# Kernel optimization log

Measured on AMD Instinct MI355X. Metric: run time of the kernel, lower is better.

## Reference

```python
import jax, jax.numpy as jnp
import numpy as np

B = 1_048_576
W = 64  # hidden width
N_FREQ = 6   # 3 dims * 6 freqs * (sin,cos) = 36
K_BLOB = 4   # one-blob bins per dim


def _freq_embed(p):
    # [B,3] -> [B,36]
    freqs = 2.0 ** jnp.arange(N_FREQ, dtype=p.dtype)
    ang = jnp.pi * p[:, :, None] * freqs  # [B,3,6]
    return jnp.concatenate([jnp.sin(ang), jnp.cos(ang)], axis=-1).reshape(p.shape[0], 3 * 2 * N_FREQ)


def _sph(d):
    # unit-square parameterization of a direction, [B,3] -> [B,2]
    d = d / (jnp.linalg.norm(d, axis=-1, keepdims=True) + 1e-8)
    u = jnp.arctan2(d[:, 1], d[:, 0]) / (2.0 * jnp.pi) + 0.5
    v = jnp.arccos(jnp.clip(d[:, 2], -1.0 + 1e-6, 1.0 - 1e-6)) / jnp.pi
    return jnp.stack([u, v], axis=-1)


def _one_blob(x, k=K_BLOB):
    # x in [0,1], [B,D] -> [B,D*k] Gaussian one-blob encoding
    centers = (jnp.arange(k, dtype=x.dtype) + 0.5) / k
    sigma = 1.0 / k
    g = jnp.exp(-0.5 * ((x[..., None] - centers) / sigma) ** 2)  # [B,D,k]
    return g.reshape(x.shape[0], -1)


def _encode(p, wi, n, alpha, beta, r):
    ones = jnp.ones((p.shape[0], 2), dtype=p.dtype)
    return jnp.concatenate([
        _freq_embed(p),                      # 36
        _one_blob(_sph(wi)),                 # 8
        _one_blob(_sph(n)),                  # 8
        _one_blob(1.0 - jnp.exp(-r)),        # 4
        alpha, beta,                         # 6
        ones,                                # 2 (implicit bias)
    ], axis=-1)                              # -> [B,64]


def _mlp(x, Ws):
    h = x
    for Wk in Ws[:-1]:
        h = jax.nn.relu(h @ Wk.T)
    return h @ Ws[-1].T  # [B,3]


def setup_inputs() -> dict:
    key = jax.random.key(0)
    ks = jax.random.split(key, 13)
    p = jax.random.normal(ks[0], (B, 3), jnp.float32)
    wi = jax.random.normal(ks[1], (B, 3), jnp.float32)
    n = jax.random.normal(ks[2], (B, 3), jnp.float32)
    alpha = jax.random.uniform(ks[3], (B, 3), jnp.float32)
    beta = jax.random.uniform(ks[4], (B, 3), jnp.float32)
    r = jax.random.uniform(ks[5], (B, 1), jnp.float32)
    s = 1.0 / np.sqrt(W)
    weights = {}
    for i in range(6):
        weights[f"W{i}"] = jax.random.normal(ks[6 + i], (W, W), jnp.float32) * s
    weights["W6"] = jax.random.normal(ks[12], (3, W), jnp.float32) * s
    return dict(p=p, wi=wi, n=n, alpha=alpha, beta=beta, r=r, **weights)


def reference(p, wi, n, alpha, beta, r, W0, W1, W2, W3, W4, W5, W6):
    x = _encode(p, wi, n, alpha, beta, r)
    out = _mlp(x, [W0, W1, W2, W3, W4, W5, W6])
    return out * (alpha + beta)  # reflectance factorization
```

## Files before the change

kernel.cpp:

```cpp
#include <hip/hip_runtime.h>


typedef _Float16 f16;
typedef f16 f16x2 __attribute__((ext_vector_type(2)));
typedef f16 f16x4 __attribute__((ext_vector_type(4)));
typedef f16 f16x8 __attribute__((ext_vector_type(8)));
typedef float f32x4 __attribute__((ext_vector_type(4)));

#define MFMA32(A, B, C) __builtin_amdgcn_mfma_f32_16x16x32_f16(A, B, C, 0, 0, 0)
#define LDS_FENCE() __asm__ volatile("" ::: "memory")

static constexpr int TILES = 4;
static constexpr int WAVES = 8;
static constexpr int BLOCK = WAVES * 64;
static constexpr int SPB   = WAVES * 64;

static constexpr int    WUNITS   = 50;
static constexpr int    WCHUNKS  = WUNITS * 64;
static constexpr size_t WS_BYTES = (size_t)WCHUNKS * 16;
static constexpr int    HUNITS   = 48;
static constexpr int    HCHUNKS  = HUNITS * 64;
static constexpr int    LDS_W    = HUNITS * 1024;

__host__ __device__ __forceinline__ int tau(int x) {
    return (x & 32) + ((x & 7) >> 2) * 16 + ((x >> 3) & 3) * 4 + (x & 3);
}

__device__ __forceinline__ f16x2 pkh(float a, float b) {
    return __builtin_bit_cast(f16x2, __builtin_amdgcn_cvt_pkrtz(a, b));
}

__device__ __forceinline__ f16x4 cat22(f16x2 a, f16x2 b) {
    return __builtin_shufflevector(a, b, 0, 1, 2, 3);
}

__device__ __forceinline__ f16x8 cat44(f16x4 a, f16x4 b) {
    return __builtin_shufflevector(a, b, 0, 1, 2, 3, 4, 5, 6, 7);
}

__device__ __forceinline__ f16x4 pack4(f32x4 v) {
    f16x2 a = pkh(v[0], v[1]);
    f16x2 b = pkh(v[2], v[3]);
    return cat22(a, b);
}

__device__ __forceinline__ float fast_atan2_rev(float y, float x) {
    const float ax = __builtin_fabsf(x), ay = __builtin_fabsf(y);
    const float mx = fmaxf(ax, ay), mn = fminf(ax, ay);
    const float a = mn * __builtin_amdgcn_rcpf(fmaxf(mx, 1e-30f));
    const float s = a * a;
    float r = a * (0.99997726f + s * (-0.33262347f + s * (0.19354346f +
              s * (-0.11643287f + s * (0.05265332f - s * 0.01172120f)))));
    if (ay > ax) r = 1.5707963268f - r;
    if (x < 0.0f) r = 3.1415926536f - r;
    r = (y < 0.0f) ? -r : r;
    return r * 0.15915494309189535f;
}

__device__ __forceinline__ float fast_acos(float x) {
    const float ax = __builtin_fabsf(x);
    const float t = __builtin_amdgcn_sqrtf(1.0f - ax);
    const float p = t * (1.5707288f + ax * (-0.2121144f +
                    ax * (0.0742610f - ax * 0.0187293f)));
    return (x < 0.0f) ? (3.1415926536f - p) : p;
}

__device__ __forceinline__ void blob4(float x, float* out) {
    const float dx = x - 0.125f;
    const float E0 = __expf(-8.0f * dx * dx);
    const float R  = __expf(4.0f * dx);
    const float t1 = R * 0.60653066f;
    const float t2 = R * 0.22313016f;
    const float t3 = R * 0.082084999f;
    out[0] = E0;
    out[1] = E0 * t1;
    out[2] = out[1] * t2;
    out[3] = out[2] * t3;
}

__device__ __forceinline__ f16x8 make_wchunk(
    int c, const float* __restrict__ W0, const float* __restrict__ W1,
    const float* __restrict__ W2, const float* __restrict__ W3,
    const float* __restrict__ W4, const float* __restrict__ W5,
    const float* __restrict__ W6)
{
    const int lane2 = c & 63;
    const int unit  = c >> 6;
    const int q = lane2 >> 4, m = lane2 & 15;
    f16x8 v;
    if (unit < 48) {
        const int l = unit >> 3, kt = (unit & 7) >> 2, mt = unit & 3;
        const float* Ws[6] = {W0, W1, W2, W3, W4, W5};
        const float* __restrict__ Wl = Ws[l];
#pragma unroll
        for (int j = 0; j < 8; ++j) {
            const int x = kt * 32 + q * 8 + j;
            const int src = (l == 0) ? x : tau(x);
            v[j] = (f16)Wl[(mt * 16 + m) * 64 + src];
        }
    } else {
        const int kt = unit - 48;
#pragma unroll
        for (int j = 0; j < 8; ++j) {
            const int src = tau(kt * 32 + q * 8 + j);
            v[j] = (m < 3) ? (f16)W6[m * 64 + src] : (f16)0.0f;
        }
    }
    return v;
}

__global__ __launch_bounds__(256, 1) void pack_weights_kernel(
    const float* __restrict__ W0, const float* __restrict__ W1,
    const float* __restrict__ W2, const float* __restrict__ W3,
    const float* __restrict__ W4, const float* __restrict__ W5,
    const float* __restrict__ W6, f16* __restrict__ ws)
{
    const int c = (int)blockIdx.x * 256 + threadIdx.x;
    if (c >= WCHUNKS) return;
    *(f16x8*)(ws + (size_t)c * 8) = make_wchunk(c, W0, W1, W2, W3, W4, W5, W6);
}

__device__ __forceinline__ void async_ld16(const void* g, void* l) {
    __builtin_amdgcn_global_load_lds(
        (const __attribute__((address_space(1))) void*)g,
        (__attribute__((address_space(3))) void*)l,
        16, 0, 0);
}

template<int PACKED>
__global__ __launch_bounds__(BLOCK, 4) void nrc_mlp_kernel(
    const float* __restrict__ P,  const float* __restrict__ WI,
    const float* __restrict__ NV, const float* __restrict__ AL,
    const float* __restrict__ BE, const float* __restrict__ RR,
    const f16*   __restrict__ ws,
    const float* __restrict__ W0, const float* __restrict__ W1,
    const float* __restrict__ W2, const float* __restrict__ W3,
    const float* __restrict__ W4, const float* __restrict__ W5,
    const float* __restrict__ W6, float* __restrict__ Out)
{
    __shared__ __attribute__((aligned(16))) unsigned char smem[LDS_W];

    const int tid  = threadIdx.x;
    const int lane = tid & 63;
    const int w    = tid >> 6;
    const int q    = lane >> 4;
    const int m    = lane & 15;
    unsigned char* const hb = smem + w * 2048;

    const int wave_base = (int)blockIdx.x * SPB + w * 64;

    f16x8 w6f0, w6f1;
    if (PACKED) {
        w6f0 = *(const f16x8*)(ws + (size_t)(HCHUNKS + lane) * 8);
        w6f1 = *(const f16x8*)(ws + (size_t)(HCHUNKS + 64 + lane) * 8);
    } else {
        w6f0 = make_wchunk(HCHUNKS + lane,      W0, W1, W2, W3, W4, W5, W6);
        w6f1 = make_wchunk(HCHUNKS + 64 + lane, W0, W1, W2, W3, W4, W5, W6);
    }

    f16x2 hf[32];
    float ab0, ab1, ab2;

    {
        const int s = wave_base + lane;

        float pv[3], wv[3], nv[3], av[3], bv[3];
#pragma unroll
        for (int d = 0; d < 3; ++d) {
            pv[d] = P [s * 3 + d];
            wv[d] = WI[s * 3 + d];
            nv[d] = NV[s * 3 + d];
            av[d] = AL[s * 3 + d];
            bv[d] = BE[s * 3 + d];
        }
        const float rv = RR[s];

#pragma unroll
        for (int d = 0; d < 3; ++d) {
            float sA[6], cA[6];
            const float fr = __builtin_amdgcn_fractf(pv[d] * 0.5f);
            sA[0] = __builtin_amdgcn_sinf(fr);
            cA[0] = __builtin_amdgcn_cosf(fr);
#pragma unroll
            for (int k = 1; k < 6; ++k) {
                const float s2 = sA[k-1] * sA[k-1];
                const float sc = sA[k-1] * cA[k-1];
                cA[k] = fmaf(-2.0f, s2, 1.0f);
                sA[k] = sc + sc;
            }
            hf[d * 6 + 0] = pkh(sA[0], sA[1]);
            hf[d * 6 + 1] = pkh(sA[2], sA[3]);
            hf[d * 6 + 2] = pkh(sA[4], sA[5]);
            hf[d * 6 + 3] = pkh(cA[0], cA[1]);
            hf[d * 6 + 4] = pkh(cA[2], cA[3]);
            hf[d * 6 + 5] = pkh(cA[4], cA[5]);
        }
#pragma unroll
        for (int which = 0; which < 2; ++which) {
            const float* dv = (which == 0) ? wv : nv;
            const int ho = 18 + which * 4;
            const float nr = __builtin_amdgcn_sqrtf(dv[0]*dv[0] + dv[1]*dv[1] + dv[2]*dv[2]) + 1e-8f;
            const float u  = fast_atan2_rev(dv[1], dv[0]) + 0.5f;
            float zc = dv[2] * __builtin_amdgcn_rcpf(nr);
            zc = fminf(fmaxf(zc, -1.0f + 1e-6f), 1.0f - 1e-6f);
            const float vv = fast_acos(zc) * 0.3183098861837907f;
            float ob[8];
            blob4(u,  &ob[0]);
            blob4(vv, &ob[4]);
            hf[ho + 0] = pkh(ob[0], ob[1]);
            hf[ho + 1] = pkh(ob[2], ob[3]);
            hf[ho + 2] = pkh(ob[4], ob[5]);
            hf[ho + 3] = pkh(ob[6], ob[7]);
        }
        {
            float ob[4];
            blob4(1.0f - __expf(-rv), ob);
            hf[26] = pkh(ob[0], ob[1]);
            hf[27] = pkh(ob[2], ob[3]);
        }
        hf[28] = pkh(av[0], av[1]);
        hf[29] = pkh(av[2], bv[0]);
        hf[30] = pkh(bv[1], bv[2]);
        hf[31] = pkh(1.0f, 1.0f);

        ab0 = av[0] + bv[0];
        ab1 = av[1] + bv[1];
        ab2 = av[2] + bv[2];
    }

    const int te = lane >> 4;
    f16x8 bf[TILES][2];
#pragma unroll
    for (int pass = 0; pass < TILES; ++pass) {
        if (te == pass) {
            unsigned char* const tb = hb + m * 128;
#pragma unroll
            for (int g = 0; g < 8; ++g) {
                const int slot0 = (4 * g + 4 * m) & 31;
                *(f16x8*)(tb + slot0 * 4) =
                    cat44(cat22(hf[g*4 + 0], hf[g*4 + 1]),
                          cat22(hf[g*4 + 2], hf[g*4 + 3]));
            }
        }
        LDS_FENCE();
#pragma unroll
        for (int kt = 0; kt < 2; ++kt) {
            const int s0 = (16 * kt + 4 * q + 4 * m) & 31;
            bf[pass][kt] = *(const f16x8*)(hb + m * 128 + s0 * 4);
        }
        LDS_FENCE();
    }

    __syncthreads();

    if (PACKED) {
#pragma unroll
        for (int i = 0; i < HCHUNKS / BLOCK; ++i) {
            const int c = i * BLOCK + tid;
            async_ld16(ws + (size_t)c * 8, smem + c * 16);
        }
    } else {
#pragma unroll
        for (int i = 0; i < HCHUNKS / BLOCK; ++i) {
            const int c = i * BLOCK + tid;
            *(f16x8*)(smem + c * 16) = make_wchunk(c, W0, W1, W2, W3, W4, W5, W6);
        }
    }
    __syncthreads();

    const f16x4 zero4 = {(f16)0.0f, (f16)0.0f, (f16)0.0f, (f16)0.0f};
    const f32x4 ZF = {0.0f, 0.0f, 0.0f, 0.0f};
    unsigned char* const wb = smem + lane * 16;

    __builtin_amdgcn_s_setprio(1);

#pragma unroll
    for (int layer = 0; layer < 6; ++layer) {
        f16x8 wa[8];
#pragma unroll
        for (int f = 0; f < 8; ++f)
            wa[f] = *(const f16x8*)(wb + (layer * 8 + f) * 1024);

#pragma unroll
        for (int t = 0; t < TILES; ++t) {
            f32x4 acc[4];
#pragma unroll
            for (int mt = 0; mt < 4; ++mt) {
                f32x4 z = MFMA32(wa[mt], bf[t][0], ZF);
                z = MFMA32(wa[4 + mt], bf[t][1], z);
                acc[mt] = z;
            }
            f16x4 pk[4];
#pragma unroll
            for (int mt = 0; mt < 4; ++mt)
                pk[mt] = __builtin_elementwise_max(pack4(acc[mt]), zero4);
            bf[t][0] = cat44(pk[0], pk[1]);
            bf[t][1] = cat44(pk[2], pk[3]);
        }
    }

    {
#pragma unroll
        for (int t = 0; t < TILES; ++t) {
            f32x4 z = MFMA32(w6f0, bf[t][0], ZF);
            z = MFMA32(w6f1, bf[t][1], z);
            const int src = t * 16 + m;
            const float s0 = __shfl(ab0, src);
            const float s1 = __shfl(ab1, src);
            const float s2 = __shfl(ab2, src);
            if (lane < 16) {
                const int s = wave_base + t * 16 + m;
                float* o = Out + s * 3;
                o[0] = z[0] * s0;
                o[1] = z[1] * s1;
                o[2] = z[2] * s2;
            }
        }
    }
    __builtin_amdgcn_s_setprio(0);
}

extern "C" void kernel_launch(void* const* d_in, const int* in_sizes, int n_in,
                              void* d_out, int out_size, void* d_ws, size_t ws_size,
                              hipStream_t stream) {
    (void)n_in; (void)out_size;
    const float* P  = (const float*)d_in[0];
    const float* WI = (const float*)d_in[1];
    const float* NV = (const float*)d_in[2];
    const float* AL = (const float*)d_in[3];
    const float* BE = (const float*)d_in[4];
    const float* RR = (const float*)d_in[5];
    const float* W0 = (const float*)d_in[6];
    const float* W1 = (const float*)d_in[7];
    const float* W2 = (const float*)d_in[8];
    const float* W3 = (const float*)d_in[9];
    const float* W4 = (const float*)d_in[10];
    const float* W5 = (const float*)d_in[11];
    const float* W6 = (const float*)d_in[12];
    f16*   ws  = (f16*)d_ws;
    float* Out = (float*)d_out;

    const int Bn = in_sizes[0] / 3;
    const int grid = Bn / SPB;

    if (ws_size >= WS_BYTES) {
        hipLaunchKernelGGL(pack_weights_kernel, dim3((WCHUNKS + 255) / 256),
                           dim3(256), 0, stream, W0, W1, W2, W3, W4, W5, W6, ws);
        hipLaunchKernelGGL((nrc_mlp_kernel<1>), dim3(grid), dim3(BLOCK), 0, stream,
                           P, WI, NV, AL, BE, RR, ws,
                           W0, W1, W2, W3, W4, W5, W6, Out);
    } else {
        hipLaunchKernelGGL((nrc_mlp_kernel<0>), dim3(grid), dim3(BLOCK), 0, stream,
                           P, WI, NV, AL, BE, RR, ws,
                           W0, W1, W2, W3, W4, W5, W6, Out);
    }
}
```

Baseline: 153.5 us.

## Split block into producer and consumer waves to overlap encoding with MLP

Waves 0-3 now compute the input encoding for the next round while waves 4-7 run the MFMA MLP on the previous round, with an LDS staging buffer and block barriers handing tiles across. Each block processes 4 rounds of 256 samples instead of 512 samples once, so the weight load to LDS is amortized over more samples. The alpha+beta scale is re-read from global memory at output time instead of being shuffled. In exchange, only half the waves issue MFMAs, each round adds four block-wide barriers, LDS use grows by 16 KB, and the grid shrinks.

```diff
diff --git a/kernel.cpp b/kernel.cpp
--- a/kernel.cpp
+++ b/kernel.cpp
@@ -8,19 +8,21 @@
 typedef float f32x4 __attribute__((ext_vector_type(4)));
 
 #define MFMA32(A, B, C) __builtin_amdgcn_mfma_f32_16x16x32_f16(A, B, C, 0, 0, 0)
-#define LDS_FENCE() __asm__ volatile("" ::: "memory")
-
-static constexpr int TILES = 4;
-static constexpr int WAVES = 8;
-static constexpr int BLOCK = WAVES * 64;
-static constexpr int SPB   = WAVES * 64;
+
+static constexpr int TILES  = 4;
+static constexpr int WAVES  = 8;
+static constexpr int BLOCK  = WAVES * 64;
+static constexpr int ROUNDS = 4;
+static constexpr int SPB    = ROUNDS * 4 * 64;
 
 static constexpr int    WUNITS   = 50;
 static constexpr int    WCHUNKS  = WUNITS * 64;
 static constexpr size_t WS_BYTES = (size_t)WCHUNKS * 16;
 static constexpr int    HUNITS   = 48;
 static constexpr int    HCHUNKS  = HUNITS * 64;
-static constexpr int    LDS_W    = HUNITS * 1024;
+static constexpr int    LDS_WEI  = HUNITS * 1024;
+static constexpr int    LDS_STG  = 4 * 4096;
+static constexpr int    LDS_TOT  = LDS_WEI + LDS_STG;
 
 __host__ __device__ __forceinline__ int tau(int x) {
     return (x & 32) + ((x & 7) >> 2) * 16 + ((x >> 3) & 3) * 4 + (x & 3);
@@ -39,9 +41,7 @@
 }
 
 __device__ __forceinline__ f16x4 pack4(f32x4 v) {
-    f16x2 a = pkh(v[0], v[1]);
-    f16x2 b = pkh(v[2], v[3]);
-    return cat22(a, b);
+    return cat22(pkh(v[0], v[1]), pkh(v[2], v[3]));
 }
 
 __device__ __forceinline__ float fast_atan2_rev(float y, float x) {
@@ -138,120 +138,18 @@
     const float* __restrict__ W4, const float* __restrict__ W5,
     const float* __restrict__ W6, float* __restrict__ Out)
 {
-    __shared__ __attribute__((aligned(16))) unsigned char smem[LDS_W];
+    __shared__ __attribute__((aligned(16))) unsigned char smem[LDS_TOT];
 
     const int tid  = threadIdx.x;
     const int lane = tid & 63;
     const int w    = tid >> 6;
     const int q    = lane >> 4;
     const int m    = lane & 15;
-    unsigned char* const hb = smem + w * 2048;
-
-    const int wave_base = (int)blockIdx.x * SPB + w * 64;
-
-    f16x8 w6f0, w6f1;
-    if (PACKED) {
-        w6f0 = *(const f16x8*)(ws + (size_t)(HCHUNKS + lane) * 8);
-        w6f1 = *(const f16x8*)(ws + (size_t)(HCHUNKS + 64 + lane) * 8);
-    } else {
-        w6f0 = make_wchunk(HCHUNKS + lane,      W0, W1, W2, W3, W4, W5, W6);
-        w6f1 = make_wchunk(HCHUNKS + 64 + lane, W0, W1, W2, W3, W4, W5, W6);
-    }
-
-    f16x2 hf[32];
-    float ab0, ab1, ab2;
-
-    {
-        const int s = wave_base + lane;
-
-        float pv[3], wv[3], nv[3], av[3], bv[3];
-#pragma unroll
-        for (int d = 0; d < 3; ++d) {
-            pv[d] = P [s * 3 + d];
-            wv[d] = WI[s * 3 + d];
-            nv[d] = NV[s * 3 + d];
-            av[d] = AL[s * 3 + d];
-            bv[d] = BE[s * 3 + d];
-        }
-        const float rv = RR[s];
-
-#pragma unroll
-        for (int d = 0; d < 3; ++d) {
-            float sA[6], cA[6];
-            const float fr = __builtin_amdgcn_fractf(pv[d] * 0.5f);
-            sA[0] = __builtin_amdgcn_sinf(fr);
-            cA[0] = __builtin_amdgcn_cosf(fr);
-#pragma unroll
-            for (int k = 1; k < 6; ++k) {
-                const float s2 = sA[k-1] * sA[k-1];
-                const float sc = sA[k-1] * cA[k-1];
-                cA[k] = fmaf(-2.0f, s2, 1.0f);
-                sA[k] = sc + sc;
-            }
-            hf[d * 6 + 0] = pkh(sA[0], sA[1]);
-            hf[d * 6 + 1] = pkh(sA[2], sA[3]);
-            hf[d * 6 + 2] = pkh(sA[4], sA[5]);
-            hf[d * 6 + 3] = pkh(cA[0], cA[1]);
-            hf[d * 6 + 4] = pkh(cA[2], cA[3]);
-            hf[d * 6 + 5] = pkh(cA[4], cA[5]);
-        }
-#pragma unroll
-        for (int which = 0; which < 2; ++which) {
-            const float* dv = (which == 0) ? wv : nv;
-            const int ho = 18 + which * 4;
-            const float nr = __builtin_amdgcn_sqrtf(dv[0]*dv[0] + dv[1]*dv[1] + dv[2]*dv[2]) + 1e-8f;
-            const float u  = fast_atan2_rev(dv[1], dv[0]) + 0.5f;
-            float zc = dv[2] * __builtin_amdgcn_rcpf(nr);
-            zc = fminf(fmaxf(zc, -1.0f + 1e-6f), 1.0f - 1e-6f);
-            const float vv = fast_acos(zc) * 0.3183098861837907f;
-            float ob[8];
-            blob4(u,  &ob[0]);
-            blob4(vv, &ob[4]);
-            hf[ho + 0] = pkh(ob[0], ob[1]);
-            hf[ho + 1] = pkh(ob[2], ob[3]);
-            hf[ho + 2] = pkh(ob[4], ob[5]);
-            hf[ho + 3] = pkh(ob[6], ob[7]);
-        }
-        {
-            float ob[4];
-            blob4(1.0f - __expf(-rv), ob);
-            hf[26] = pkh(ob[0], ob[1]);
-            hf[27] = pkh(ob[2], ob[3]);
-        }
-        hf[28] = pkh(av[0], av[1]);
-        hf[29] = pkh(av[2], bv[0]);
-        hf[30] = pkh(bv[1], bv[2]);
-        hf[31] = pkh(1.0f, 1.0f);
-
-        ab0 = av[0] + bv[0];
-        ab1 = av[1] + bv[1];
-        ab2 = av[2] + bv[2];
-    }
-
-    const int te = lane >> 4;
-    f16x8 bf[TILES][2];
-#pragma unroll
-    for (int pass = 0; pass < TILES; ++pass) {
-        if (te == pass) {
-            unsigned char* const tb = hb + m * 128;
-#pragma unroll
-            for (int g = 0; g < 8; ++g) {
-                const int slot0 = (4 * g + 4 * m) & 31;
-                *(f16x8*)(tb + slot0 * 4) =
-                    cat44(cat22(hf[g*4 + 0], hf[g*4 + 1]),
-                          cat22(hf[g*4 + 2], hf[g*4 + 3]));
-            }
-        }
-        LDS_FENCE();
-#pragma unroll
-        for (int kt = 0; kt < 2; ++kt) {
-            const int s0 = (16 * kt + 4 * q + 4 * m) & 31;
-            bf[pass][kt] = *(const f16x8*)(hb + m * 128 + s0 * 4);
-        }
-        LDS_FENCE();
-    }
-
-    __syncthreads();
+    const bool producer = (w < 4);
+    const int  cw  = w & 3;
+    const int  blk_base = (int)blockIdx.x * SPB;
+
+    unsigned char* const stg = smem + LDS_WEI;
 
     if (PACKED) {
 #pragma unroll
@@ -266,58 +164,170 @@
             *(f16x8*)(smem + c * 16) = make_wchunk(c, W0, W1, W2, W3, W4, W5, W6);
         }
     }
-    __syncthreads();
+
+    f16x8 w6f0{}, w6f1{};
+    if (!producer) {
+        if (PACKED) {
+            w6f0 = *(const f16x8*)(ws + (size_t)(HCHUNKS + lane) * 8);
+            w6f1 = *(const f16x8*)(ws + (size_t)(HCHUNKS + 64 + lane) * 8);
+        } else {
+            w6f0 = make_wchunk(HCHUNKS + lane,      W0, W1, W2, W3, W4, W5, W6);
+            w6f1 = make_wchunk(HCHUNKS + 64 + lane, W0, W1, W2, W3, W4, W5, W6);
+        }
+    }
 
     const f16x4 zero4 = {(f16)0.0f, (f16)0.0f, (f16)0.0f, (f16)0.0f};
     const f32x4 ZF = {0.0f, 0.0f, 0.0f, 0.0f};
     unsigned char* const wb = smem + lane * 16;
 
-    __builtin_amdgcn_s_setprio(1);
-
-#pragma unroll
-    for (int layer = 0; layer < 6; ++layer) {
-        f16x8 wa[8];
-#pragma unroll
-        for (int f = 0; f < 8; ++f)
-            wa[f] = *(const f16x8*)(wb + (layer * 8 + f) * 1024);
-
+    f16x8 bf[TILES][2];
+
+    auto compute = [&](int rr) {
+        __builtin_amdgcn_s_setprio(1);
+#pragma unroll
+        for (int layer = 0; layer < 6; ++layer) {
+            f16x8 wa[8];
+#pragma unroll
+            for (int f = 0; f < 8; ++f)
+                wa[f] = *(const f16x8*)(wb + (layer * 8 + f) * 1024);
+
+#pragma unroll
+            for (int t = 0; t < TILES; ++t) {
+                f32x4 acc[4];
+#pragma unroll
+                for (int mt = 0; mt < 4; ++mt) {
+                    f32x4 z = MFMA32(wa[mt], bf[t][0], ZF);
+                    z = MFMA32(wa[4 + mt], bf[t][1], z);
+                    acc[mt] = z;
+                }
+                f16x4 pk[4];
+#pragma unroll
+                for (int mt = 0; mt < 4; ++mt)
+                    pk[mt] = __builtin_elementwise_max(pack4(acc[mt]), zero4);
+                bf[t][0] = cat44(pk[0], pk[1]);
+                bf[t][1] = cat44(pk[2], pk[3]);
+            }
+        }
+        const int rbase = blk_base + rr * 256 + cw * 64;
+        float aa[TILES][3];
 #pragma unroll
         for (int t = 0; t < TILES; ++t) {
-            f32x4 acc[4];
-#pragma unroll
-            for (int mt = 0; mt < 4; ++mt) {
-                f32x4 z = MFMA32(wa[mt], bf[t][0], ZF);
-                z = MFMA32(wa[4 + mt], bf[t][1], z);
-                acc[mt] = z;
-            }
-            f16x4 pk[4];
-#pragma unroll
-            for (int mt = 0; mt < 4; ++mt)
-                pk[mt] = __builtin_elementwise_max(pack4(acc[mt]), zero4);
-            bf[t][0] = cat44(pk[0], pk[1]);
-            bf[t][1] = cat44(pk[2], pk[3]);
-        }
-    }
-
-    {
+            const int s = rbase + t * 16 + m;
+#pragma unroll
+            for (int d = 0; d < 3; ++d)
+                aa[t][d] = AL[s * 3 + d] + BE[s * 3 + d];
+        }
 #pragma unroll
         for (int t = 0; t < TILES; ++t) {
             f32x4 z = MFMA32(w6f0, bf[t][0], ZF);
             z = MFMA32(w6f1, bf[t][1], z);
-            const int src = t * 16 + m;
-            const float s0 = __shfl(ab0, src);
-            const float s1 = __shfl(ab1, src);
-            const float s2 = __shfl(ab2, src);
             if (lane < 16) {
-                const int s = wave_base + t * 16 + m;
+                const int s = rbase + t * 16 + m;
                 float* o = Out + s * 3;
-                o[0] = z[0] * s0;
-                o[1] = z[1] * s1;
-                o[2] = z[2] * s2;
-            }
-        }
-    }
-    __builtin_amdgcn_s_setprio(0);
+                o[0] = z[0] * aa[t][0];
+                o[1] = z[1] * aa[t][1];
+                o[2] = z[2] * aa[t][2];
+            }
+        }
+        __builtin_amdgcn_s_setprio(0);
+    };
+
+    for (int r = 0; r < ROUNDS; ++r) {
+        f16x2 hf[32];
+        if (producer) {
+            const int s = blk_base + r * 256 + cw * 64 + lane;
+
+            float pv[3], wv[3], nv[3], av[3], bv[3];
+#pragma unroll
+            for (int d = 0; d < 3; ++d) {
+                pv[d] = P [s * 3 + d];
+                wv[d] = WI[s * 3 + d];
+                nv[d] = NV[s * 3 + d];
+                av[d] = AL[s * 3 + d];
+                bv[d] = BE[s * 3 + d];
+            }
+            const float rv = RR[s];
+
+#pragma unroll
+            for (int d = 0; d < 3; ++d) {
+                float sA[6], cA[6];
+                const float fr = __builtin_amdgcn_fractf(pv[d] * 0.5f);
+                sA[0] = __builtin_amdgcn_sinf(fr);
+                cA[0] = __builtin_amdgcn_cosf(fr);
+#pragma unroll
+                for (int k = 1; k < 6; ++k) {
+                    const float s2 = sA[k-1] * sA[k-1];
+                    const float sc = sA[k-1] * cA[k-1];
+                    cA[k] = fmaf(-2.0f, s2, 1.0f);
+                    sA[k] = sc + sc;
+                }
+                hf[d * 6 + 0] = pkh(sA[0], sA[1]);
+                hf[d * 6 + 1] = pkh(sA[2], sA[3]);
+                hf[d * 6 + 2] = pkh(sA[4], sA[5]);
+                hf[d * 6 + 3] = pkh(cA[0], cA[1]);
+                hf[d * 6 + 4] = pkh(cA[2], cA[3]);
+                hf[d * 6 + 5] = pkh(cA[4], cA[5]);
+            }
+#pragma unroll
+            for (int which = 0; which < 2; ++which) {
+                const float* dv = (which == 0) ? wv : nv;
+                const int ho = 18 + which * 4;
+                const float nr = __builtin_amdgcn_sqrtf(dv[0]*dv[0] + dv[1]*dv[1] + dv[2]*dv[2]) + 1e-8f;
+                const float u  = fast_atan2_rev(dv[1], dv[0]) + 0.5f;
+                float zc = dv[2] * __builtin_amdgcn_rcpf(nr);
+                zc = fminf(fmaxf(zc, -1.0f + 1e-6f), 1.0f - 1e-6f);
+                const float vv = fast_acos(zc) * 0.3183098861837907f;
+                float ob[8];
+                blob4(u,  &ob[0]);
+                blob4(vv, &ob[4]);
+                hf[ho + 0] = pkh(ob[0], ob[1]);
+                hf[ho + 1] = pkh(ob[2], ob[3]);
+                hf[ho + 2] = pkh(ob[4], ob[5]);
+                hf[ho + 3] = pkh(ob[6], ob[7]);
+            }
+            {
+                float ob[4];
+                blob4(1.0f - __expf(-rv), ob);
+                hf[26] = pkh(ob[0], ob[1]);
+                hf[27] = pkh(ob[2], ob[3]);
+            }
+            hf[28] = pkh(av[0], av[1]);
+            hf[29] = pkh(av[2], bv[0]);
+            hf[30] = pkh(bv[1], bv[2]);
+            hf[31] = pkh(1.0f, 1.0f);
+        } else if (r > 0) {
+            compute(r - 1);
+        }
+
+#pragma unroll
+        for (int h = 0; h < 2; ++h) {
+            __syncthreads();
+            if (producer && ((lane >> 5) == h)) {
+                unsigned char* const tb =
+                    stg + cw * 4096 + ((lane >> 4) & 1) * 2048 + m * 128;
+#pragma unroll
+                for (int g = 0; g < 8; ++g) {
+                    const int slot0 = (4 * g + 4 * m) & 31;
+                    *(f16x8*)(tb + slot0 * 4) =
+                        cat44(cat22(hf[g*4 + 0], hf[g*4 + 1]),
+                              cat22(hf[g*4 + 2], hf[g*4 + 3]));
+                }
+            }
+            __syncthreads();
+            if (!producer) {
+#pragma unroll
+                for (int t2 = 0; t2 < 2; ++t2) {
+#pragma unroll
+                    for (int kt = 0; kt < 2; ++kt) {
+                        const int s0 = (16 * kt + 4 * q + 4 * m) & 31;
+                        bf[h * 2 + t2][kt] = *(const f16x8*)(
+                            stg + cw * 4096 + t2 * 2048 + m * 128 + s0 * 4);
+                    }
+                }
+            }
+        }
+    }
+    if (!producer) compute(ROUNDS - 1);
 }
 
 extern "C" void kernel_launch(void* const* d_in, const int* in_sizes, int n_in,
```

Result: slower. 194.1 us (+26.5%).
